# Performance work log

Measured on AMD Instinct MI355X. Metric: run time of the kernel, lower is better.

## Reference

```python
import jax, jax.numpy as jnp
import numpy as np

B, N, F, H, A, T = 4, 256, 64, 256, 16, 3


def setup_inputs() -> dict:
    key = jax.random.key(0)
    ks = jax.random.split(key, 18)
    s = 0.05
    rn = lambda k, shp: jax.random.normal(k, shp, dtype=jnp.float32) * s
    return {
        "node_features": jax.random.normal(ks[0], (B, N, F), dtype=jnp.float32),
        "adjacency": jax.random.randint(ks[1], (B, N, N), 0, 2).astype(jnp.int32),
        # preprocess MLP: F->H->H
        "pre_W1": rn(ks[2], (F, H)), "pre_b1": jnp.zeros((H,), jnp.float32),
        "pre_W2": rn(ks[3], (H, H)), "pre_b2": jnp.zeros((H,), jnp.float32),
        # message MLP: 2H->H->H
        "msg_W1": rn(ks[4], (2 * H, H)), "msg_b1": jnp.zeros((H,), jnp.float32),
        "msg_W2": rn(ks[5], (H, H)), "msg_b2": jnp.zeros((H,), jnp.float32),
        # GRUCell params (jax layout [in, 3H]; gate order r,z,n like torch)
        "gru_Wih": rn(ks[6], (H, 3 * H)), "gru_Whh": rn(ks[7], (H, 3 * H)),
        "gru_bih": jnp.zeros((3 * H,), jnp.float32), "gru_bhh": jnp.zeros((3 * H,), jnp.float32),
        # readout MLP: H->H->A
        "ro_W1": rn(ks[8], (H, H)), "ro_b1": jnp.zeros((H,), jnp.float32),
        "ro_W2": rn(ks[9], (H, A)), "ro_b2": jnp.zeros((A,), jnp.float32),
    }


def reference(node_features, adjacency, pre_W1, pre_b1, pre_W2, pre_b2,
              msg_W1, msg_b1, msg_W2, msg_b2,
              gru_Wih, gru_Whh, gru_bih, gru_bhh,
              ro_W1, ro_b1, ro_W2, ro_b2):
    adj = adjacency.astype(node_features.dtype)  # [B,N,N]
    # preprocess: Linear-ReLU-Linear
    h = jnp.maximum(node_features @ pre_W1 + pre_b1, 0.0) @ pre_W2 + pre_b2  # [B,N,H]

    W1_i, W1_j = msg_W1[:H], msg_W1[H:]  # concat([h_i,h_j]) @ W1 == h_i@W1_i + h_j@W1_j
    for _ in range(T):
        hi = h @ W1_i  # [B,N,H] receiver part
        hj = h @ W1_j  # [B,N,H] sender part
        e = jnp.maximum(hi[:, :, None, :] + hj[:, None, :, :] + msg_b1, 0.0)  # [B,N,N,H]
        m = e @ msg_W2 + msg_b2  # [B,N,N,H] messages
        agg = jnp.einsum('bijh,bij->bih', m, adj)  # mask + sum over senders j
        # GRUCell(input=agg, hidden=h), torch gate order (r, z, n)
        gi = agg @ gru_Wih + gru_bih  # [B,N,3H]
        gh = h @ gru_Whh + gru_bhh
        ir, iz, inn = jnp.split(gi, 3, axis=-1)
        hr, hz, hn = jnp.split(gh, 3, axis=-1)
        r = jax.nn.sigmoid(ir + hr)
        z = jax.nn.sigmoid(iz + hz)
        n = jnp.tanh(inn + r * hn)
        h = (1.0 - z) * n + z * h

    g = jnp.sum(h, axis=1)  # [B,H] graph readout
    q = jnp.maximum(g @ ro_W1 + ro_b1, 0.0) @ ro_W2 + ro_b2  # [B,A]
    return q
```

## Files before the change

### kernel.cpp

```cpp
#include <hip/hip_runtime.h>
#include <hip/hip_bf16.h>


typedef unsigned short ushort_t;
typedef short bf8_t __attribute__((ext_vector_type(8)));
typedef float f4_t  __attribute__((ext_vector_type(4)));

#define BN_ROWS 1024

#define UB_NFB    0
#define UB_PW1T   65536
#define UB_PW2T   81920
#define UB_WCATT  147456
#define UB_WGT    475136
#define UB_H2     917504
#define UB_EHAT2  1441792

#define F_PREB1   1015808
#define F_PREB2   1016064
#define F_BCAT    1016320
#define F_BIH     1017600
#define F_ROW1    1018368
#define F_ROB1    1083904
#define F_ROW2    1084160
#define F_ROB2    1088256
#define F_H       1088272
#define F_HCAT    1350416
#define F_FLAG    2661136
#define F_GCNT    2661140

#define CVa 65536
#define CVb 81920
#define CVc 147456
#define CVd 475136
#define CV_TOTAL 547600
#define NCONV 1070

__device__ __forceinline__ float bf2f(ushort_t u) {
    return __uint_as_float(((unsigned int)u) << 16);
}
__device__ __forceinline__ ushort_t f2b(float v) {
    __hip_bfloat16 b = __float2bfloat16(v);
    return *reinterpret_cast<ushort_t*>(&b);
}
__device__ __forceinline__ float relu(float v) { return v < 0.f ? 0.f : v; }
__device__ __forceinline__ float ld(const void* p, int i, int isf32) {
    return isf32 ? ((const float*)p)[i] : bf2f(((const ushort_t*)p)[i]);
}

__global__ __launch_bounds__(256) void convwg_kernel(
    const void* nf, const void* preW1, const void* preb1, const void* preW2, const void* preb2,
    const void* msgW1, const void* msgb1, const void* msgW2, const void* msgb2,
    const void* gruWih, const void* gruWhh, const void* grubih, const void* grubhh,
    const void* roW1, const void* rob1, const void* roW2, const void* rob2,
    float* __restrict__ w)
{
    __shared__ float w2s[4 * 256];
    __shared__ int cnt;
    const int t = threadIdx.x;
    ushort_t* wb = (ushort_t*)w;

    if (t == 0) cnt = 0;
    __syncthreads();
    {
        const ushort_t* nf0 = (const ushort_t*)nf;
        int bad = 0;
        for (int i = 0; i < 8; ++i) {
            ushort_t u = nf0[(t * 8 + i) * 2];
            int ex = (u >> 7) & 0xFF;
            if ((u & 0x7fff) != 0 && (ex < 100 || ex > 140)) bad++;
        }
        atomicAdd(&cnt, bad);
    }
    __syncthreads();
    const int f32 = (cnt > 512) ? 1 : 0;

    if (blockIdx.x == 0) {
        if (t < 4) ((int*)(w + F_GCNT))[t] = 0;
        if (t == 4) *(int*)(w + F_FLAG) = f32;
    }

    if (blockIdx.x < NCONV) {
        const int e0 = (blockIdx.x * 256 + t) * 2;
#pragma unroll
        for (int u2 = 0; u2 < 2; ++u2) {
            int e = e0 + u2;
            if (e >= CV_TOTAL) break;
            if (e < CVa) {
                wb[UB_NFB + e] = f2b(ld(nf, e, f32));
            } else if (e < CVb) {
                int i = e - CVa; int n = i >> 6, k = i & 63;
                wb[UB_PW1T + i] = f2b(ld(preW1, k * 256 + n, f32));
            } else if (e < CVc) {
                int i = e - CVb; int n = i >> 8, k = i & 255;
                wb[UB_PW2T + i] = f2b(ld(preW2, k * 256 + n, f32));
            } else if (e < CVd) {
                int i = e - CVc; int n = i >> 8, k = i & 255;
                float v;
                if (n < 256)      v = ld(msgW1, k * 256 + n, f32);
                else if (n < 512) v = ld(msgW1, (256 + k) * 256 + (n - 256), f32);
                else              v = ld(gruWhh, k * 768 + (n - 512), f32);
                wb[UB_WCATT + i] = f2b(v);
            } else {
                int f = e - CVd;
                float v;
                if (f < 256)        v = ld(preb1, f, f32);
                else if (f < 512)   v = ld(preb2, f - 256, f32);
                else if (f < 1792) {
                    int c = f - 512;
                    if (c < 256)      v = ld(msgb1, c, f32);
                    else if (c < 512) v = 0.f;
                    else              v = ld(grubhh, c - 512, f32);
                }
                else if (f < 2560)  v = ld(grubih, f - 1792, f32);
                else if (f < 68096) v = ld(roW1, f - 2560, f32);
                else if (f < 68352) v = ld(rob1, f - 68096, f32);
                else if (f < 72448) v = ld(roW2, f - 68352, f32);
                else                v = ld(rob2, f - 72448, f32);
                w[F_PREB1 + f] = v;
            }
        }
        return;
    }

    const int wt = blockIdx.x - NCONV;
    const int p0 = (wt % 3) * 256;
    const int k0 = (wt / 3) * 4;
    for (int i = t; i < 4 * 256; i += 256) {
        int r = i >> 8, n = i & 255;
        int krow = k0 + r;
        float v;
        if (krow < 256)       v = ld(msgW2, krow * 256 + n, f32);
        else if (krow == 256) v = ld(msgb2, n, f32);
        else                  v = 0.f;
        w2s[i] = v;
    }
    __syncthreads();
    const int p = p0 + t;
    float acc4[4] = {};
    for (int n0 = 0; n0 < 256; n0 += 32) {
        float wv[32];
#pragma unroll
        for (int i = 0; i < 32; ++i)
            wv[i] = ld(gruWih, (n0 + i) * 768 + p, f32);
#pragma unroll
        for (int r = 0; r < 4; ++r) {
            float acc = acc4[r];
#pragma unroll
            for (int q = 0; q < 8; ++q) {
                f4_t w4 = *(const f4_t*)&w2s[r * 256 + n0 + q * 4];
                acc += w4[0] * wv[q * 4 + 0] + w4[1] * wv[q * 4 + 1]
                     + w4[2] * wv[q * 4 + 2] + w4[3] * wv[q * 4 + 3];
            }
            acc4[r] = acc;
        }
    }
#pragma unroll
    for (int r = 0; r < 4; ++r) {
        int krow = k0 + r;
        ushort_t hi = f2b(acc4[r]);
        ushort_t lo = f2b(acc4[r] - bf2f(hi));
        wb[UB_WGT + p * 576 + krow] = hi;
        wb[UB_WGT + p * 576 + 288 + krow] = lo;
    }
}

__global__ __launch_bounds__(256) void prenet_kernel(float* __restrict__ w)
{
    __shared__ ushort_t As[32 * 64];
    __shared__ ushort_t Xs[32 * 256];
    __shared__ ushort_t Bs[256 * 32];
    ushort_t* wb = (ushort_t*)w;
    const int t = threadIdx.x;
    const int wave = t >> 6, lane = t & 63;
    const int ln = lane & 15, quad = lane >> 4;
    const int wr = (wave & 1) * 16, wc = (wave >> 1) * 128;
    const int xcd = blockIdx.x & 7;
    const int gph = xcd >> 1;
    const int lidx = ((blockIdx.x >> 3) << 1) | (xcd & 1);
    const int rbase = gph * 256 + lidx * 32;
    const int srow = t >> 2, skc = (t & 3) << 3;

    {
        int row = t >> 3, kc = (t & 7) << 3;
        *(bf8_t*)(&As[row * 64 + kc]) =
            *(const bf8_t*)(&wb[UB_NFB + (rbase + row) * 64 + kc]);
    }

    f4_t acc[8] = {};
    for (int k0 = 0; k0 < 64; k0 += 32) {
        __syncthreads();
#pragma unroll
        for (int rr = 0; rr < 4; ++rr) {
            int n = srow + 64 * rr;
            *(bf8_t*)(&Bs[n * 32 + skc]) =
                *(const bf8_t*)(&wb[UB_PW1T + n * 64 + k0 + skc]);
        }
        __syncthreads();
        bf8_t af = *(const bf8_t*)(&As[(wr + ln) * 64 + k0 + quad * 8]);
#pragma unroll
        for (int n = 0; n < 8; ++n) {
            bf8_t bfr = *(const bf8_t*)(&Bs[(wc + n * 16 + ln) * 32 + quad * 8]);
            acc[n] = __builtin_amdgcn_mfma_f32_16x16x32_bf16(af, bfr, acc[n], 0, 0, 0);
        }
    }
    __syncthreads();
#pragma unroll
    for (int n = 0; n < 8; ++n) {
        int col = wc + n * 16 + ln;
        float bb = w[F_PREB1 + col];
#pragma unroll
        for (int r = 0; r < 4; ++r) {
            int row = wr + quad * 4 + r;
            Xs[row * 256 + col] = f2b(relu(acc[n][r] + bb));
        }
        acc[n] = (f4_t){0.f, 0.f, 0.f, 0.f};
    }
    __syncthreads();

    for (int k0 = 0; k0 < 256; k0 += 32) {
        __syncthreads();
#pragma unroll
        for (int rr = 0; rr < 4; ++rr) {
            int n = srow + 64 * rr;
            *(bf8_t*)(&Bs[n * 32 + skc]) =
                *(const bf8_t*)(&wb[UB_PW2T + n * 256 + k0 + skc]);
        }
        __syncthreads();
        bf8_t af = *(const bf8_t*)(&Xs[(wr + ln) * 256 + k0 + quad * 8]);
#pragma unroll
        for (int n = 0; n < 8; ++n) {
            bf8_t bfr = *(const bf8_t*)(&Bs[(wc + n * 16 + ln) * 32 + quad * 8]);
            acc[n] = __builtin_amdgcn_mfma_f32_16x16x32_bf16(af, bfr, acc[n], 0, 0, 0);
        }
    }
#pragma unroll
    for (int n = 0; n < 8; ++n) {
        int col = wc + n * 16 + ln;
        float bb = w[F_PREB2 + col];
#pragma unroll
        for (int r = 0; r < 4; ++r) {
            int grow = rbase + wr + quad * 4 + r;
            float v = acc[n][r] + bb;
            w[F_H + grow * 256 + col] = v;
            ushort_t hi = f2b(v);
            wb[UB_H2 + grow * 512 + col] = hi;
            wb[UB_H2 + grow * 512 + 256 + col] = f2b(v - bf2f(hi));
        }
    }
}

#define HLD 104
__global__ __launch_bounds__(256) void hcat_kernel(float* __restrict__ w)
{
    __shared__ ushort_t As[32 * HLD];
    __shared__ ushort_t Bs[128 * HLD];
    ushort_t* wb = (ushort_t*)w;
    const ushort_t* A  = wb + UB_H2;
    const ushort_t* Bt = wb + UB_WCATT;
    const int t = threadIdx.x;
    const int wave = t >> 6, lane = t & 63;
    const int ln = lane & 15, quad = lane >> 4;
    const int xcd = blockIdx.x & 7;
    const int gph = xcd >> 1;
    const int lidx = ((blockIdx.x >> 3) << 1) | (xcd & 1);
    const int bm = gph * 256 + (lidx >> 2) * 32;
    const int bn = (lidx & 3) * 128;
    const int wm = (wave >> 1) * 16, wn = (wave & 1) * 64;

    const int arow = t >> 3, akc = (t & 7) << 3;
    const int agoff = (bm + arow) * 512 + akc;
    const int aloff = arow * HLD + akc;
    int bgoff[4], bloff[4];
#pragma unroll
    for (int i = 0; i < 4; ++i) {
        int slot = i * 256 + t;
        int brow = slot >> 3, bkc = (slot & 7) << 3;
        bgoff[i] = (bn + brow) * 256 + bkc;
        bloff[i] = brow * HLD + bkc;
    }

    f4_t acc[4] = {};
    bf8_t ra, rb[4];

    ra = *(const bf8_t*)(&A[agoff]);
#pragma unroll
    for (int i = 0; i < 4; ++i)
        rb[i] = *(const bf8_t*)(&Bt[bgoff[i]]);

    for (int ks = 0; ks < 8; ++ks) {
        __syncthreads();
        *(bf8_t*)(&As[aloff]) = ra;
#pragma unroll
        for (int i = 0; i < 4; ++i)
            *(bf8_t*)(&Bs[bloff[i]]) = rb[i];
        __syncthreads();
        if (ks < 7) {
            int k0 = (ks + 1) * 64;
            int kb = k0 & 255;
            ra = *(const bf8_t*)(&A[agoff + k0]);
#pragma unroll
            for (int i = 0; i < 4; ++i)
                rb[i] = *(const bf8_t*)(&Bt[bgoff[i] + kb]);
        }
#pragma unroll
        for (int kk = 0; kk < 2; ++kk) {
            bf8_t af = *(const bf8_t*)(&As[(wm + ln) * HLD + kk * 32 + quad * 8]);
#pragma unroll
            for (int ni = 0; ni < 4; ++ni) {
                bf8_t bfr = *(const bf8_t*)(&Bs[(wn + ni * 16 + ln) * HLD + kk * 32 + quad * 8]);
                acc[ni] = __builtin_amdgcn_mfma_f32_16x16x32_bf16(af, bfr, acc[ni], 0, 0, 0);
            }
        }
    }

#pragma unroll
    for (int ni = 0; ni < 4; ++ni) {
        int col = bn + wn + ni * 16 + ln;
        float bb = w[F_BCAT + col];
#pragma unroll
        for (int r = 0; r < 4; ++r) {
            int row = bm + wm + quad * 4 + r;
            w[F_HCAT + row * 512 + col] = acc[ni][r] + bb;
        }
    }
}

__global__ __launch_bounds__(256) void msg_kernel(
    const float* __restrict__ hcat,
    const int*   __restrict__ adj,
    ushort_t* __restrict__ ehat)
{
    const int xcd = blockIdx.x & 7;
    const int gph = xcd >> 1;
    const int idx = ((blockIdx.x >> 3) << 1) | (xcd & 1);
    const int row = gph * 256 + idx;
    const int t = threadIdx.x;
    __shared__ int ej[256];
    __shared__ int ecnt;
    if (t == 0) ecnt = 0;
    __syncthreads();
    if (adj[row * 256 + t]) { int p = atomicAdd(&ecnt, 1); ej[p] = t; }
    const float hi = hcat[row * 512 + t];
    const float* hjb = hcat + gph * 256 * 512 + 256;
    __syncthreads();
    const int ne = ecnt;
    float acc = 0.f;
#pragma unroll 4
    for (int p = 0; p < ne; ++p) {
        int j = ej[p];
        acc += relu(hi + hjb[j * 512 + t]);
    }
    ushort_t h16 = f2b(acc);
    ushort_t l16 = f2b(acc - bf2f(h16));
    ushort_t* er = ehat + row * 576;
    er[t] = h16;
    er[288 + t] = l16;
    if (t < 32) {
        er[256 + t] = f2b(t == 0 ? (float)ne : 0.f);
        er[544 + t] = 0;
    }
}

#define GLD 104
template<int FINAL>
__global__ __launch_bounds__(256) void gigru_kernel(float* __restrict__ w,
                                                    void* __restrict__ out)
{
    __shared__ ushort_t As[16 * GLD];
    __shared__ ushort_t Bs[192 * GLD];
    __shared__ float gl[256];
    __shared__ float t1[256];
    __shared__ int donef;
    ushort_t* wb = (ushort_t*)w;
    const int t = threadIdx.x;
    const int wave = t >> 6, lane = t & 63;
    const int ln = lane & 15, quad = lane >> 4;
    const int xcd = blockIdx.x & 7;
    const int gph = xcd >> 1;
    const int lidx = ((blockIdx.x >> 3) << 1) | (xcd & 1);
    const int cg = lidx & 3;
    const int rg = gph * 16 + (lidx >> 2);
    const int rbase = rg * 16;

    const int aval = (t < 192);
    const int arow = t / 12, akc = (t % 12) * 8;
    const int agoff = (rbase + arow) * 576 + akc;
    const int aloff = arow * GLD + akc;
    int bgoff[9], bloff[9];
#pragma unroll
    for (int i = 0; i < 9; ++i) {
        int slot = i * 256 + t;
        int brow = slot / 12, bkc = (slot % 12) * 8;
        int wrow = (brow >> 6) * 256 + cg * 64 + (brow & 63);
        bgoff[i] = wrow * 576 + bkc;
        bloff[i] = brow * GLD + bkc;
    }
    const ushort_t* Ehp = wb + UB_EHAT2;
    const ushort_t* Bp  = wb + UB_WGT;

    f4_t acc[3] = {};
    {
        bf8_t ra, rb[9];
        if (aval) ra = *(const bf8_t*)(&Ehp[agoff]);
#pragma unroll
        for (int i = 0; i < 9; ++i)
            rb[i] = *(const bf8_t*)(&Bp[bgoff[i]]);

        for (int ks = 0; ks < 9; ++ks) {
            __syncthreads();
            if (aval) *(bf8_t*)(&As[aloff]) = ra;
#pragma unroll
            for (int i = 0; i < 9; ++i)
                *(bf8_t*)(&Bs[bloff[i]]) = rb[i];
            __syncthreads();
            if (ks < 8) {
                int k0 = (ks + 1) * 96;
                int ka = (k0 < 576) ? k0 : k0 - 576;
                int kb = (k0 < 288) ? k0 : k0 - 288;
                if (aval) ra = *(const bf8_t*)(&Ehp[agoff + ka]);
#pragma unroll
                for (int i = 0; i < 9; ++i)
                    rb[i] = *(const bf8_t*)(&Bp[bgoff[i] + kb]);
            }
#pragma unroll
            for (int kk = 0; kk < 3; ++kk) {
                bf8_t af = *(const bf8_t*)(&As[ln * GLD + kk * 32 + quad * 8]);
#pragma unroll
                for (int n = 0; n < 3; ++n) {
                    int fn = wave + n * 4;
                    bf8_t bfr = *(const bf8_t*)(&Bs[(fn * 16 + ln) * GLD + kk * 32 + quad * 8]);
                    acc[n] = __builtin_amdgcn_mfma_f32_16x16x32_bf16(af, bfr, acc[n], 0, 0, 0);
                }
            }
        }
    }

    const int aval2 = (t < 128);
    const int arow2 = t >> 3, akc2 = (t & 7) << 3;
    const int agoff2 = (rbase + arow2) * 512 + akc2;
    const int aloff2 = arow2 * GLD + akc2;
    int bgoff2[6], bloff2[6];
#pragma unroll
    for (int i = 0; i < 6; ++i) {
        int slot = i * 256 + t;
        int brow = slot >> 3, bkc = (slot & 7) << 3;
        int wrow = 512 + (brow >> 6) * 256 + cg * 64 + (brow & 63);
        bgoff2[i] = wrow * 256 + bkc;
        bloff2[i] = brow * GLD + bkc;
    }
    const ushort_t* Hp = wb + UB_H2;
    const ushort_t* Wp = wb + UB_WCATT;

    f4_t acch[3] = {};
    {
        bf8_t ra, rb[6];
        if (aval2) ra = *(const bf8_t*)(&Hp[agoff2]);
#pragma unroll
        for (int i = 0; i < 6; ++i)
            rb[i] = *(const bf8_t*)(&Wp[bgoff2[i]]);

        for (int ks = 0; ks < 8; ++ks) {
            __syncthreads();
            if (aval2) *(bf8_t*)(&As[aloff2]) = ra;
#pragma unroll
            for (int i = 0; i < 6; ++i)
                *(bf8_t*)(&Bs[bloff2[i]]) = rb[i];
            __syncthreads();
            if (ks < 7) {
                int k0 = (ks + 1) * 64;
                int kb = k0 & 255;
                if (aval2) ra = *(const bf8_t*)(&Hp[agoff2 + k0]);
#pragma unroll
                for (int i = 0; i < 6; ++i)
                    rb[i] = *(const bf8_t*)(&Wp[bgoff2[i] + kb]);
            }
#pragma unroll
            for (int kk = 0; kk < 2; ++kk) {
                bf8_t af = *(const bf8_t*)(&As[ln * GLD + kk * 32 + quad * 8]);
#pragma unroll
                for (int n = 0; n < 3; ++n) {
                    int fn = wave + n * 4;
                    bf8_t bfr = *(const bf8_t*)(&Bs[(fn * 16 + ln) * GLD + kk * 32 + quad * 8]);
                    acch[n] = __builtin_amdgcn_mfma_f32_16x16x32_bf16(af, bfr, acch[n], 0, 0, 0);
                }
            }
        }
    }

    {
        const int col = cg * 64 + wave * 16 + ln;
        float bi_r = w[F_BIH + col];
        float bi_z = w[F_BIH + 256 + col];
        float bi_n = w[F_BIH + 512 + col];
        float bh_r = w[F_BCAT + 512 + col];
        float bh_z = w[F_BCAT + 768 + col];
        float bh_n = w[F_BCAT + 1024 + col];
#pragma unroll
        for (int r = 0; r < 4; ++r) {
            int row = rbase + quad * 4 + r;
            float ir = acc[0][r] + bi_r;
            float iz = acc[1][r] + bi_z;
            float in = acc[2][r] + bi_n;
            float hr = acch[0][r] + bh_r;
            float hz = acch[1][r] + bh_z;
            float hn = acch[2][r] + bh_n;
            float rg_ = 1.f / (1.f + __expf(-(ir + hr)));
            float z   = 1.f / (1.f + __expf(-(iz + hz)));
            float nn  = tanhf(in + rg_ * hn);
            float ho = w[F_H + row * 256 + col];
            float hv = (1.f - z) * nn + z * ho;
            w[F_H + row * 256 + col] = hv;
            if (!FINAL) {
                ushort_t hb = f2b(hv);
                wb[UB_H2 + row * 512 + col] = hb;
                wb[UB_H2 + row * 512 + 256 + col] = f2b(hv - bf2f(hb));
            }
        }
    }

    if (FINAL) {
        const int g = gph;
        __syncthreads();
        if (t == 0) {
            __threadfence();
            int prev = atomicAdd((int*)(w + F_GCNT) + g, 1);
            donef = (prev == 63);
        }
        __syncthreads();
        if (!donef) return;
        __threadfence();

        const float* hb = w + F_H + g * 256 * 256;
        float s = 0.f;
        for (int n = 0; n < 256; ++n) s += hb[n * 256 + t];
        gl[t] = s;
        __syncthreads();
        float acc1 = w[F_ROB1 + t];
        for (int k = 0; k < 256; ++k) acc1 += gl[k] * w[F_ROW1 + k * 256 + t];
        t1[t] = relu(acc1);
        __syncthreads();
        if (t < 16) {
            float q = w[F_ROB2 + t];
            for (int k = 0; k < 256; ++k) q += t1[k] * w[F_ROW2 + k * 16 + t];
            if (*(const int*)(w + F_FLAG)) ((float*)out)[g * 16 + t] = q;
            else ((__hip_bfloat16*)out)[g * 16 + t] = __float2bfloat16(q);
        }
    }
}

extern "C" void kernel_launch(void* const* d_in, const int* in_sizes, int n_in,
                              void* d_out, int out_size, void* d_ws, size_t ws_size,
                              hipStream_t stream) {
    float* w = (float*)d_ws;
    ushort_t* wb = (ushort_t*)d_ws;

    static const int dictSz[18]  = {65536,262144,16384,256,65536,256,131072,256,65536,256,
                                    196608,196608,768,768,65536,256,4096,16};
    static const int alphaSz[18] = {262144,196608,196608,768,768,131072,65536,256,256,
                                    65536,16384,65536,256,256,65536,4096,256,16};
    static const int alphaPos[18] = {9,0,10,12,11,13,5,7,6,8,2,1,4,3,14,16,15,17};
    bool dictOK = true, alphaOK = true;
    for (int i = 0; i < 18 && i < n_in; ++i) {
        if (in_sizes[i] != dictSz[i])  dictOK = false;
        if (in_sizes[i] != alphaSz[i]) alphaOK = false;
    }
    const void* P[18];
    for (int l = 0; l < 18; ++l) P[l] = d_in[(!dictOK && alphaOK) ? alphaPos[l] : l];
    const int* adj = (const int*)P[1];

    convwg_kernel<<<NCONV + 216, 256, 0, stream>>>(
        P[0], P[2], P[3], P[4], P[5], P[6], P[7], P[8], P[9],
        P[10], P[11], P[12], P[13], P[14], P[15], P[16], P[17], w);

    prenet_kernel<<<32, 256, 0, stream>>>(w);

    for (int it = 0; it < 3; ++it) {
        hcat_kernel<<<128, 256, 0, stream>>>(w);
        msg_kernel<<<BN_ROWS, 256, 0, stream>>>(w + F_HCAT, adj, wb + UB_EHAT2);
        if (it < 2)
            gigru_kernel<0><<<256, 256, 0, stream>>>(w, d_out);
        else
            gigru_kernel<1><<<256, 256, 0, stream>>>(w, d_out);
    }
}
```

Before: 257.6 us.

## Precompute adjacency edge lists once and drop fp32 hidden-state buffer

Adds 64 blocks to the conversion kernel that compact each adjacency row into a ushort neighbor list and count, so the three msg_kernel passes read the precomputed list instead of rebuilding it with shared atomics. It also removes the fp32 copy of h: the GRU kernel reconstructs the old h from its split bf16 hi/lo pair and ping-pongs between two such buffers, which avoids an in-place read/write hazard. This cuts global traffic and per-iteration atomic work, at the cost of extra workspace and a slightly different fp32 reconstruction of h.

```diff
diff --git a/kernel.cpp b/kernel.cpp
--- a/kernel.cpp
+++ b/kernel.cpp
@@ -24,8 +24,10 @@
 #define F_ROB1    1083904
 #define F_ROW2    1084160
 #define F_ROB2    1088256
-#define F_H       1088272
+#define EJ_U      2176544
+#define F_ECNT    1219344
 #define F_HCAT    1350416
+#define UB_H2B    3749408
 #define F_FLAG    2661136
 #define F_GCNT    2661140
 
@@ -53,10 +55,11 @@
     const void* msgW1, const void* msgb1, const void* msgW2, const void* msgb2,
     const void* gruWih, const void* gruWhh, const void* grubih, const void* grubhh,
     const void* roW1, const void* rob1, const void* roW2, const void* rob2,
-    float* __restrict__ w)
+    const int* __restrict__ adj, float* __restrict__ w)
 {
     __shared__ float w2s[4 * 256];
     __shared__ int cnt;
+    __shared__ int cnt2;
     const int t = threadIdx.x;
     ushort_t* wb = (ushort_t*)w;
 
@@ -123,45 +126,64 @@
         return;
     }
 
-    const int wt = blockIdx.x - NCONV;
-    const int p0 = (wt % 3) * 256;
-    const int k0 = (wt / 3) * 4;
-    for (int i = t; i < 4 * 256; i += 256) {
-        int r = i >> 8, n = i & 255;
-        int krow = k0 + r;
-        float v;
-        if (krow < 256)       v = ld(msgW2, krow * 256 + n, f32);
-        else if (krow == 256) v = ld(msgb2, n, f32);
-        else                  v = 0.f;
-        w2s[i] = v;
-    }
-    __syncthreads();
-    const int p = p0 + t;
-    float acc4[4] = {};
-    for (int n0 = 0; n0 < 256; n0 += 32) {
-        float wv[32];
-#pragma unroll
-        for (int i = 0; i < 32; ++i)
-            wv[i] = ld(gruWih, (n0 + i) * 768 + p, f32);
+    if (blockIdx.x < NCONV + 216) {
+        const int wt = blockIdx.x - NCONV;
+        const int p0 = (wt % 3) * 256;
+        const int k0 = (wt / 3) * 4;
+        for (int i = t; i < 4 * 256; i += 256) {
+            int r = i >> 8, n = i & 255;
+            int krow = k0 + r;
+            float v;
+            if (krow < 256)       v = ld(msgW2, krow * 256 + n, f32);
+            else if (krow == 256) v = ld(msgb2, n, f32);
+            else                  v = 0.f;
+            w2s[i] = v;
+        }
+        __syncthreads();
+        const int p = p0 + t;
+        float acc4[4] = {};
+        for (int n0 = 0; n0 < 256; n0 += 32) {
+            float wv[32];
+#pragma unroll
+            for (int i = 0; i < 32; ++i)
+                wv[i] = ld(gruWih, (n0 + i) * 768 + p, f32);
+#pragma unroll
+            for (int r = 0; r < 4; ++r) {
+                float acc = acc4[r];
+#pragma unroll
+                for (int q = 0; q < 8; ++q) {
+                    f4_t w4 = *(const f4_t*)&w2s[r * 256 + n0 + q * 4];
+                    acc += w4[0] * wv[q * 4 + 0] + w4[1] * wv[q * 4 + 1]
+                         + w4[2] * wv[q * 4 + 2] + w4[3] * wv[q * 4 + 3];
+                }
+                acc4[r] = acc;
+            }
+        }
 #pragma unroll
         for (int r = 0; r < 4; ++r) {
-            float acc = acc4[r];
-#pragma unroll
-            for (int q = 0; q < 8; ++q) {
-                f4_t w4 = *(const f4_t*)&w2s[r * 256 + n0 + q * 4];
-                acc += w4[0] * wv[q * 4 + 0] + w4[1] * wv[q * 4 + 1]
-                     + w4[2] * wv[q * 4 + 2] + w4[3] * wv[q * 4 + 3];
-            }
-            acc4[r] = acc;
-        }
-    }
-#pragma unroll
-    for (int r = 0; r < 4; ++r) {
-        int krow = k0 + r;
-        ushort_t hi = f2b(acc4[r]);
-        ushort_t lo = f2b(acc4[r] - bf2f(hi));
-        wb[UB_WGT + p * 576 + krow] = hi;
-        wb[UB_WGT + p * 576 + 288 + krow] = lo;
+            int krow = k0 + r;
+            ushort_t hi = f2b(acc4[r]);
+            ushort_t lo = f2b(acc4[r] - bf2f(hi));
+            wb[UB_WGT + p * 576 + krow] = hi;
+            wb[UB_WGT + p * 576 + 288 + krow] = lo;
+        }
+        return;
+    }
+
+    {
+        const int r0 = (blockIdx.x - (NCONV + 216)) * 16;
+        for (int i = 0; i < 16; ++i) {
+            const int row = r0 + i;
+            __syncthreads();
+            if (t == 0) cnt2 = 0;
+            __syncthreads();
+            if (adj[row * 256 + t]) {
+                int p = atomicAdd(&cnt2, 1);
+                wb[EJ_U + row * 256 + p] = (ushort_t)t;
+            }
+            __syncthreads();
+            if (t == 0) ((int*)(w + F_ECNT))[row] = cnt2;
+        }
     }
 }
 
@@ -242,7 +264,6 @@
         for (int r = 0; r < 4; ++r) {
             int grow = rbase + wr + quad * 4 + r;
             float v = acc[n][r] + bb;
-            w[F_H + grow * 256 + col] = v;
             ushort_t hi = f2b(v);
             wb[UB_H2 + grow * 512 + col] = hi;
             wb[UB_H2 + grow * 512 + 256 + col] = f2b(v - bf2f(hi));
@@ -251,12 +272,12 @@
 }
 
 #define HLD 104
-__global__ __launch_bounds__(256) void hcat_kernel(float* __restrict__ w)
+__global__ __launch_bounds__(256) void hcat_kernel(float* __restrict__ w, int hoff)
 {
     __shared__ ushort_t As[32 * HLD];
     __shared__ ushort_t Bs[128 * HLD];
     ushort_t* wb = (ushort_t*)w;
-    const ushort_t* A  = wb + UB_H2;
+    const ushort_t* A  = wb + hoff;
     const ushort_t* Bt = wb + UB_WCATT;
     const int t = threadIdx.x;
     const int wave = t >> 6, lane = t & 63;
@@ -326,34 +347,30 @@
     }
 }
 
-__global__ __launch_bounds__(256) void msg_kernel(
-    const float* __restrict__ hcat,
-    const int*   __restrict__ adj,
-    ushort_t* __restrict__ ehat)
+__global__ __launch_bounds__(256) void msg_kernel(float* __restrict__ w)
 {
+    ushort_t* wb = (ushort_t*)w;
+    const float* hcat = w + F_HCAT;
     const int xcd = blockIdx.x & 7;
     const int gph = xcd >> 1;
     const int idx = ((blockIdx.x >> 3) << 1) | (xcd & 1);
     const int row = gph * 256 + idx;
     const int t = threadIdx.x;
-    __shared__ int ej[256];
-    __shared__ int ecnt;
-    if (t == 0) ecnt = 0;
-    __syncthreads();
-    if (adj[row * 256 + t]) { int p = atomicAdd(&ecnt, 1); ej[p] = t; }
+    __shared__ ushort_t ejs[256];
+    ejs[t] = wb[EJ_U + row * 256 + t];
+    const int ne = ((const int*)(w + F_ECNT))[row];
     const float hi = hcat[row * 512 + t];
     const float* hjb = hcat + gph * 256 * 512 + 256;
     __syncthreads();
-    const int ne = ecnt;
     float acc = 0.f;
 #pragma unroll 4
     for (int p = 0; p < ne; ++p) {
-        int j = ej[p];
+        int j = ejs[p];
         acc += relu(hi + hjb[j * 512 + t]);
     }
     ushort_t h16 = f2b(acc);
     ushort_t l16 = f2b(acc - bf2f(h16));
-    ushort_t* er = ehat + row * 576;
+    ushort_t* er = wb + UB_EHAT2 + row * 576;
     er[t] = h16;
     er[288 + t] = l16;
     if (t < 32) {
@@ -365,7 +382,8 @@
 #define GLD 104
 template<int FINAL>
 __global__ __launch_bounds__(256) void gigru_kernel(float* __restrict__ w,
-                                                    void* __restrict__ out)
+                                                    void* __restrict__ out,
+                                                    int rdoff, int wroff)
 {
     __shared__ ushort_t As[16 * GLD];
     __shared__ ushort_t Bs[192 * GLD];
@@ -449,7 +467,7 @@
         bgoff2[i] = wrow * 256 + bkc;
         bloff2[i] = brow * GLD + bkc;
     }
-    const ushort_t* Hp = wb + UB_H2;
+    const ushort_t* Hp = wb + rdoff;
     const ushort_t* Wp = wb + UB_WCATT;
 
     f4_t acch[3] = {};
@@ -508,14 +526,12 @@
             float rg_ = 1.f / (1.f + __expf(-(ir + hr)));
             float z   = 1.f / (1.f + __expf(-(iz + hz)));
             float nn  = tanhf(in + rg_ * hn);
-            float ho = w[F_H + row * 256 + col];
+            float ho = bf2f(wb[rdoff + row * 512 + col])
+                     + bf2f(wb[rdoff + row * 512 + 256 + col]);
             float hv = (1.f - z) * nn + z * ho;
-            w[F_H + row * 256 + col] = hv;
-            if (!FINAL) {
-                ushort_t hb = f2b(hv);
-                wb[UB_H2 + row * 512 + col] = hb;
-                wb[UB_H2 + row * 512 + 256 + col] = f2b(hv - bf2f(hb));
-            }
+            ushort_t hb = f2b(hv);
+            wb[wroff + row * 512 + col] = hb;
+            wb[wroff + row * 512 + 256 + col] = f2b(hv - bf2f(hb));
         }
     }
 
@@ -531,9 +547,10 @@
         if (!donef) return;
         __threadfence();
 
-        const float* hb = w + F_H + g * 256 * 256;
+        const ushort_t* h2r = wb + wroff + g * 256 * 512;
         float s = 0.f;
-        for (int n = 0; n < 256; ++n) s += hb[n * 256 + t];
+        for (int n = 0; n < 256; ++n)
+            s += bf2f(h2r[n * 512 + t]) + bf2f(h2r[n * 512 + 256 + t]);
         gl[t] = s;
         __syncthreads();
         float acc1 = w[F_ROB1 + t];
@@ -553,7 +570,6 @@
                               void* d_out, int out_size, void* d_ws, size_t ws_size,
                               hipStream_t stream) {
     float* w = (float*)d_ws;
-    ushort_t* wb = (ushort_t*)d_ws;
 
     static const int dictSz[18]  = {65536,262144,16384,256,65536,256,131072,256,65536,256,
                                     196608,196608,768,768,65536,256,4096,16};
@@ -569,18 +585,22 @@
     for (int l = 0; l < 18; ++l) P[l] = d_in[(!dictOK && alphaOK) ? alphaPos[l] : l];
     const int* adj = (const int*)P[1];
 
-    convwg_kernel<<<NCONV + 216, 256, 0, stream>>>(
+    convwg_kernel<<<NCONV + 216 + 64, 256, 0, stream>>>(
         P[0], P[2], P[3], P[4], P[5], P[6], P[7], P[8], P[9],
-        P[10], P[11], P[12], P[13], P[14], P[15], P[16], P[17], w);
+        P[10], P[11], P[12], P[13], P[14], P[15], P[16], P[17], adj, w);
 
     prenet_kernel<<<32, 256, 0, stream>>>(w);
 
-    for (int it = 0; it < 3; ++it) {
-        hcat_kernel<<<128, 256, 0, stream>>>(w);
-        msg_kernel<<<BN_ROWS, 256, 0, stream>>>(w + F_HCAT, adj, wb + UB_EHAT2);
-        if (it < 2)
-            gigru_kernel<0><<<256, 256, 0, stream>>>(w, d_out);
-        else
-            gigru_kernel<1><<<256, 256, 0, stream>>>(w, d_out);
-    }
-}
+    const int hA = UB_H2, hB = UB_H2B;
+    hcat_kernel<<<128, 256, 0, stream>>>(w, hA);
+    msg_kernel<<<BN_ROWS, 256, 0, stream>>>(w);
+    gigru_kernel<0><<<256, 256, 0, stream>>>(w, d_out, hA, hB);
+
+    hcat_kernel<<<128, 256, 0, stream>>>(w, hB);
+    msg_kernel<<<BN_ROWS, 256, 0, stream>>>(w);
+    gigru_kernel<0><<<256, 256, 0, stream>>>(w, d_out, hB, hA);
+
+    hcat_kernel<<<128, 256, 0, stream>>>(w, hA);
+    msg_kernel<<<BN_ROWS, 256, 0, stream>>>(w);
+    gigru_kernel<1><<<256, 256, 0, stream>>>(w, d_out, hA, hB);
+}
```

After: 261.8 us. About the same (+1.6%).
